# Kernel optimization log

Hardware: AMD Instinct MI355X
Metric: run time of the kernel (lower is better)

## Reference

```python
import jax, jax.numpy as jnp
import numpy as np

NUM_STAGES = 2
DE_NEIGHBORS = 3

def _square_distance(a, b):
    # a: [B,N,3], b: [B,S,3] -> [B,N,S] squared euclidean distances
    return (jnp.sum(a * a, axis=-1)[:, :, None]
            + jnp.sum(b * b, axis=-1)[:, None, :]
            - 2.0 * jnp.einsum('bnc,bsc->bns', a, b))

def _propagate(xyz1, xyz2, points1, points2, k):
    # xyz1:[B,N,3] fine, xyz2:[B,S,3] coarse, points1:[B,D1,N], points2:[B,D2,S]
    p2 = jnp.transpose(points2, (0, 2, 1))  # [B,S,D2]
    B, N, _ = xyz1.shape
    S = xyz2.shape[1]
    if S == 1:
        interp = jnp.broadcast_to(p2, (B, N, p2.shape[-1]))
    else:
        d = _square_distance(xyz1, xyz2)              # [B,N,S]
        neg_top, idx = jax.lax.top_k(-d, k)           # k smallest distances
        dists = -neg_top                              # [B,N,k]
        recip = 1.0 / (dists + 1e-8)
        weight = recip / jnp.sum(recip, axis=2, keepdims=True)  # [B,N,k]
        # gather neighbor features: [B,N,k,D2]
        gathered = jnp.take_along_axis(p2[:, None, :, :], idx[..., None], axis=2)
        interp = jnp.sum(gathered * weight[..., None], axis=2)  # [B,N,D2]
    if points1 is not None:
        p1 = jnp.transpose(points1, (0, 2, 1))        # [B,N,D1]
        new = jnp.concatenate([p1, interp], axis=-1)
    else:
        new = interp
    return jnp.transpose(new, (0, 2, 1))              # [B,D1+D2,N]

def setup_inputs() -> dict:
    key = jax.random.key(0)
    ks = jax.random.split(key, 6)
    return {
        'xyz0': jax.random.normal(ks[0], (4, 8192, 3), dtype=jnp.float32),
        'xyz1': jax.random.normal(ks[1], (4, 2048, 3), dtype=jnp.float32),
        'xyz2': jax.random.normal(ks[2], (4, 512, 3), dtype=jnp.float32),
        'x0': jax.random.normal(ks[3], (4, 128, 8192), dtype=jnp.float32),
        'x1': jax.random.normal(ks[4], (4, 256, 2048), dtype=jnp.float32),
        'x2': jax.random.normal(ks[5], (4, 512, 512), dtype=jnp.float32),
    }

def reference(xyz0, xyz1, xyz2, x0, x1, x2):
    # original forward reverses the lists; emulate with pre-reversed lists
    xyz_list = [xyz2, xyz1, xyz0]   # coarse -> fine
    x_list = [x2, x1, x0]
    x = x_list[0]
    for i in range(NUM_STAGES):
        x = _propagate(xyz_list[i + 1], xyz_list[i], x_list[i + 1], x, DE_NEIGHBORS)
    return x  # [4, 896, 8192]
```

## Files before the change

### kernel.cpp

```cpp
#include <hip/hip_runtime.h>

#define BIG 3.0e38f

__device__ __forceinline__ void insert3(float d, int s,
                                        float& d0, float& d1, float& d2,
                                        int& i0, int& i1, int& i2) {
    const bool b0 = d < d0;
    const bool b1 = d < d1;
    const bool b2 = d < d2;
    d2 = b1 ? d1 : (b2 ? d : d2);
    i2 = b1 ? i1 : (b2 ? s : i2);
    d1 = b0 ? d0 : (b1 ? d : d1);
    i1 = b0 ? i0 : (b1 ? s : i1);
    d0 = b0 ? d : d0;
    i0 = b0 ? s : i0;
}

template <int S>
__device__ void knn_tile(const float* __restrict__ xyzF, const float* __restrict__ xyzC,
                         int N, int b, int nb,
                         int* __restrict__ idx, float* __restrict__ w,
                         void* smem) {
    constexpr int SPC = S / 8;
    float4* sc  = (float4*)smem;
    float*  smd = (float*)((char*)smem + S * 16);
    int*    smi = (int*)((char*)smem + S * 16 + 3072);
    const int tid = threadIdx.x;

    for (int i = tid; i < S; i += 256) {
        const float x = xyzC[(b * S + i) * 3 + 0];
        const float y = xyzC[(b * S + i) * 3 + 1];
        const float z = xyzC[(b * S + i) * 3 + 2];
        sc[i] = make_float4(x, y, z, x * x + y * y + z * z);
    }
    __syncthreads();

    const int q  = tid & 31;
    const int sp = tid >> 5;
    const int n  = nb + q;
    const float ax = xyzF[(b * N + n) * 3 + 0];
    const float ay = xyzF[(b * N + n) * 3 + 1];
    const float az = xyzF[(b * N + n) * 3 + 2];
    const float an = ax * ax + ay * ay + az * az;

    float d0 = BIG, d1 = BIG, d2 = BIG;
    int i0 = 0, i1 = 0, i2 = 0;
    const int s0 = sp * SPC;
#pragma unroll 8
    for (int s = s0; s < s0 + SPC; ++s) {
        const float4 p = sc[s];
        const float t = ax * p.x + ay * p.y + az * p.z;
        const float d = an + p.w - 2.0f * t;
        insert3(d, s, d0, d1, d2, i0, i1, i2);
    }

    smd[tid * 3 + 0] = d0; smi[tid * 3 + 0] = i0;
    smd[tid * 3 + 1] = d1; smi[tid * 3 + 1] = i1;
    smd[tid * 3 + 2] = d2; smi[tid * 3 + 2] = i2;
    __syncthreads();

    if (tid < 32) {
        float e0 = BIG, e1 = BIG, e2 = BIG;
        int j0 = 0, j1 = 0, j2 = 0;
#pragma unroll
        for (int ch = 0; ch < 8; ++ch) {
#pragma unroll
            for (int k = 0; k < 3; ++k) {
                insert3(smd[(ch * 32 + tid) * 3 + k], smi[(ch * 32 + tid) * 3 + k],
                        e0, e1, e2, j0, j1, j2);
            }
        }
        const float r0 = 1.0f / (e0 + 1e-8f);
        const float r1 = 1.0f / (e1 + 1e-8f);
        const float r2 = 1.0f / (e2 + 1e-8f);
        const float rs = r0 + r1 + r2;
        const int nn = nb + tid;
        idx[(b * 3 + 0) * N + nn] = j0;
        idx[(b * 3 + 1) * N + nn] = j1;
        idx[(b * 3 + 2) * N + nn] = j2;
        w[(b * 3 + 0) * N + nn] = r0 / rs;
        w[(b * 3 + 1) * N + nn] = r1 / rs;
        w[(b * 3 + 2) * N + nn] = r2 / rs;
    }
}

__device__ void transpose_tile(const float* __restrict__ in, float* __restrict__ out,
                               int C, int N, int OS,
                               int b, int nb, int cb, void* smem) {
    float (*s)[65] = (float (*)[65])smem;
    const int lo = threadIdx.x & 63;
    const int r  = threadIdx.x >> 6;
#pragma unroll
    for (int i = 0; i < 16; ++i) {
        const int cl = r + 4 * i;
        s[cl][lo] = in[((size_t)b * C + cb + cl) * N + nb + lo];
    }
    __syncthreads();
#pragma unroll
    for (int i = 0; i < 16; ++i) {
        const int pl = r + 4 * i;
        out[((size_t)b * N + nb + pl) * OS + cb + lo] = s[lo][pl];
    }
}

__global__ __launch_bounds__(256) void k1_stage(const float* __restrict__ xyz0,
                                                const float* __restrict__ xyz1,
                                                const float* __restrict__ xyz2,
                                                const float* __restrict__ x0,
                                                const float* __restrict__ x1,
                                                const float* __restrict__ x2,
                                                float* __restrict__ x1P,
                                                float* __restrict__ x2P,
                                                int* __restrict__ idx1,
                                                float* __restrict__ w1,
                                                int* __restrict__ idx2,
                                                float* __restrict__ w2,
                                                float* __restrict__ out) {
    __shared__ float4 smem4[2432];
    const int id = blockIdx.x;
    if (id < 1024) {
        const int b  = id >> 8;
        const int nb = (id & 255) * 32;
        knn_tile<2048>(xyz0, xyz1, 8192, b, nb, idx2, w2, smem4);
    } else if (id < 1280) {
        const int r  = id - 1024;
        const int b  = r >> 6;
        const int nb = (r & 63) * 32;
        knn_tile<512>(xyz1, xyz2, 2048, b, nb, idx1, w1, smem4);
    } else if (id < 1536) {
        const int r  = id - 1280;
        const int b  = r >> 6;
        const int nb = (r & 7) * 64;
        const int cb = ((r >> 3) & 7) * 64;
        transpose_tile(x2, x2P, 512, 512, 512, b, nb, cb, smem4);
    } else if (id < 2048) {
        const int r  = id - 1536;
        const int b  = r >> 7;
        const int nb = (r & 31) * 64;
        const int cb = ((r >> 5) & 3) * 64;
        transpose_tile(x1, x1P, 256, 2048, 256, b, nb, cb, smem4);
    } else {
        const int r  = id - 2048;
        const int b  = r >> 6;
        const int lb = r & 63;
        const float4* src = (const float4*)x0;
        float4* dst = (float4*)out;
#pragma unroll
        for (int t = 0; t < 16; ++t) {
            const int i = lb * 4096 + t * 256 + threadIdx.x;
            dst[(size_t)b * (896 * 2048) + i] = src[(size_t)b * (128 * 2048) + i];
        }
    }
}

__global__ __launch_bounds__(256) void final_fused(const float* __restrict__ x1P,
                                                   const float* __restrict__ x2P,
                                                   const int* __restrict__ idx1,
                                                   const float* __restrict__ w1,
                                                   const int* __restrict__ idx2,
                                                   const float* __restrict__ w2,
                                                   float* __restrict__ out) {
    __shared__ float tile[64][65];
    __shared__ int   sj[9][64];
    __shared__ float sw[9][64];
    const int b = blockIdx.y;
    const int id = blockIdx.x;
    const int ntile = (id & 7) * 16 + ((id >> 3) & 15);
    const int ctile = id >> 7;
    const int nb = ntile * 64;
    const int tid = threadIdx.x;

    if (ctile < 4) {
        if (tid < 64) {
#pragma unroll
            for (int k = 0; k < 3; ++k) {
                sj[k][tid] = idx2[(b * 3 + k) * 8192 + nb + tid];
                sw[k][tid] = w2[(b * 3 + k) * 8192 + nb + tid];
            }
        }
        __syncthreads();
        const int cb = ctile * 64;
        {
            const int c = tid & 63, r = tid >> 6;
            const float* xb = x1P + (size_t)b * 2048 * 256 + cb + c;
#pragma unroll
            for (int i = 0; i < 16; ++i) {
                const int p = r + 4 * i;
                const float v = sw[0][p] * xb[(size_t)sj[0][p] * 256]
                              + sw[1][p] * xb[(size_t)sj[1][p] * 256]
                              + sw[2][p] * xb[(size_t)sj[2][p] * 256];
                tile[p][c] = v;
            }
        }
        __syncthreads();
        {
            const int p = tid & 63, r = tid >> 6;
#pragma unroll
            for (int i = 0; i < 16; ++i) {
                const int cl = r + 4 * i;
                out[((size_t)b * 896 + 128 + cb + cl) * 8192 + nb + p] = tile[p][cl];
            }
        }
    } else {
        if (tid < 64) {
            const int n = nb + tid;
#pragma unroll
            for (int k = 0; k < 3; ++k) {
                const int   j  = idx2[(b * 3 + k) * 8192 + n];
                const float wk = w2[(b * 3 + k) * 8192 + n];
#pragma unroll
                for (int m = 0; m < 3; ++m) {
                    sj[k * 3 + m][tid] = idx1[(b * 3 + m) * 2048 + j];
                    sw[k * 3 + m][tid] = wk * w1[(b * 3 + m) * 2048 + j];
                }
            }
        }
        __syncthreads();
        const int cb = (ctile - 4) * 64;
        {
            const int c = tid & 63, r = tid >> 6;
            const float* xb = x2P + (size_t)b * 512 * 512 + cb + c;
#pragma unroll
            for (int i = 0; i < 16; ++i) {
                const int p = r + 4 * i;
                float v = 0.0f;
#pragma unroll
                for (int j = 0; j < 9; ++j) {
                    v += sw[j][p] * xb[(size_t)sj[j][p] * 512];
                }
                tile[p][c] = v;
            }
        }
        __syncthreads();
        {
            const int p = tid & 63, r = tid >> 6;
#pragma unroll
            for (int i = 0; i < 16; ++i) {
                const int cl = r + 4 * i;
                out[((size_t)b * 896 + 384 + cb + cl) * 8192 + nb + p] = tile[p][cl];
            }
        }
    }
}

extern "C" void kernel_launch(void* const* d_in, const int* in_sizes, int n_in,
                              void* d_out, int out_size, void* d_ws, size_t ws_size,
                              hipStream_t stream) {
    const float* xyz0 = (const float*)d_in[0];
    const float* xyz1 = (const float*)d_in[1];
    const float* xyz2 = (const float*)d_in[2];
    const float* x0   = (const float*)d_in[3];
    const float* x1   = (const float*)d_in[4];
    const float* x2   = (const float*)d_in[5];
    float* out = (float*)d_out;

    char* ws = (char*)d_ws;
    float* x1P  = (float*)(ws + 0);
    float* x2P  = (float*)(ws + 8388608);
    int*   idx1 = (int*)(ws + 12582912);
    float* w1   = (float*)(ws + 12681216);
    int*   idx2 = (int*)(ws + 12779520);
    float* w2   = (float*)(ws + 13172736);

    k1_stage<<<dim3(2304), 256, 0, stream>>>(xyz0, xyz1, xyz2, x0, x1, x2,
                                             x1P, x2P, idx1, w1, idx2, w2, out);
    final_fused<<<dim3(1536, 4), 256, 0, stream>>>(x1P, x2P, idx1, w1, idx2, w2, out);
}
```

Baseline: 213.9 us.

## Interleave stage-1 block roles, remap final blocks per XCD, use nontemporal stores

The first kernel interleaves heavy KNN blocks with light transpose and copy blocks (4 of every 9) so long-running work is spread across the whole grid rather than concentrated at the front. The final kernel flattens the grid and maps each batch onto a pair of XCDs, so the gathered x1P/x2P tiles for that batch stay within those XCDs' L2 caches. Neighbor index and weight loading now uses 192 threads instead of 64. Output writes and the x0 copy use nontemporal loads and stores to avoid polluting cache. The added index arithmetic (divisions by 9 and 12) is minor, and the XCD mapping relies on round-robin block dispatch across the eight XCDs.

```diff
diff --git a/kernel.cpp b/kernel.cpp
--- a/kernel.cpp
+++ b/kernel.cpp
@@ -1,6 +1,8 @@
 #include <hip/hip_runtime.h>
 
 #define BIG 3.0e38f
+
+typedef float vf4 __attribute__((ext_vector_type(4)));
 
 __device__ __forceinline__ void insert3(float d, int s,
                                         float& d0, float& d1, float& d2,
@@ -118,37 +120,43 @@
                                                 float* __restrict__ out) {
     __shared__ float4 smem4[2432];
     const int id = blockIdx.x;
-    if (id < 1024) {
-        const int b  = id >> 8;
-        const int nb = (id & 255) * 32;
+    const int g  = id / 9;
+    const int r9 = id - g * 9;
+    if (r9 < 4) {
+        const int kid = g * 4 + r9;
+        const int b  = kid >> 8;
+        const int nb = (kid & 255) * 32;
         knn_tile<2048>(xyz0, xyz1, 8192, b, nb, idx2, w2, smem4);
-    } else if (id < 1280) {
-        const int r  = id - 1024;
-        const int b  = r >> 6;
-        const int nb = (r & 63) * 32;
-        knn_tile<512>(xyz1, xyz2, 2048, b, nb, idx1, w1, smem4);
-    } else if (id < 1536) {
-        const int r  = id - 1280;
-        const int b  = r >> 6;
-        const int nb = (r & 7) * 64;
-        const int cb = ((r >> 3) & 7) * 64;
-        transpose_tile(x2, x2P, 512, 512, 512, b, nb, cb, smem4);
-    } else if (id < 2048) {
-        const int r  = id - 1536;
-        const int b  = r >> 7;
-        const int nb = (r & 31) * 64;
-        const int cb = ((r >> 5) & 3) * 64;
-        transpose_tile(x1, x1P, 256, 2048, 256, b, nb, cb, smem4);
     } else {
-        const int r  = id - 2048;
-        const int b  = r >> 6;
-        const int lb = r & 63;
-        const float4* src = (const float4*)x0;
-        float4* dst = (float4*)out;
-#pragma unroll
-        for (int t = 0; t < 16; ++t) {
-            const int i = lb * 4096 + t * 256 + threadIdx.x;
-            dst[(size_t)b * (896 * 2048) + i] = src[(size_t)b * (128 * 2048) + i];
+        const int mid = g * 5 + (r9 - 4);
+        if (mid < 256) {
+            const int b  = mid >> 6;
+            const int nb = (mid & 63) * 32;
+            knn_tile<512>(xyz1, xyz2, 2048, b, nb, idx1, w1, smem4);
+        } else if (mid < 512) {
+            const int r  = mid - 256;
+            const int b  = r >> 6;
+            const int nb = (r & 7) * 64;
+            const int cb = ((r >> 3) & 7) * 64;
+            transpose_tile(x2, x2P, 512, 512, 512, b, nb, cb, smem4);
+        } else if (mid < 1024) {
+            const int r  = mid - 512;
+            const int b  = r >> 7;
+            const int nb = (r & 31) * 64;
+            const int cb = ((r >> 5) & 3) * 64;
+            transpose_tile(x1, x1P, 256, 2048, 256, b, nb, cb, smem4);
+        } else {
+            const int r  = mid - 1024;
+            const int b  = r >> 6;
+            const int lb = r & 63;
+            const vf4* src = (const vf4*)x0;
+            vf4* dst = (vf4*)out;
+#pragma unroll
+            for (int t = 0; t < 16; ++t) {
+                const int i = lb * 4096 + t * 256 + threadIdx.x;
+                const vf4 v = __builtin_nontemporal_load(&src[(size_t)b * (128 * 2048) + i]);
+                __builtin_nontemporal_store(v, &dst[(size_t)b * (896 * 2048) + i]);
+            }
         }
     }
 }
@@ -163,20 +171,20 @@
     __shared__ float tile[64][65];
     __shared__ int   sj[9][64];
     __shared__ float sw[9][64];
-    const int b = blockIdx.y;
-    const int id = blockIdx.x;
-    const int ntile = (id & 7) * 16 + ((id >> 3) & 15);
-    const int ctile = id >> 7;
-    const int nb = ntile * 64;
+    const int id  = blockIdx.x;
+    const int xcd = id & 7;
+    const int b   = xcd >> 1;
+    const int local = ((id >> 3) << 1) | (xcd & 1);
+    const int ntile = local / 12;
+    const int ctile = local - ntile * 12;
+    const int nb  = ntile * 64;
     const int tid = threadIdx.x;
 
     if (ctile < 4) {
-        if (tid < 64) {
-#pragma unroll
-            for (int k = 0; k < 3; ++k) {
-                sj[k][tid] = idx2[(b * 3 + k) * 8192 + nb + tid];
-                sw[k][tid] = w2[(b * 3 + k) * 8192 + nb + tid];
-            }
+        if (tid < 192) {
+            const int p = tid & 63, k = tid >> 6;
+            sj[k][p] = idx2[(b * 3 + k) * 8192 + nb + p];
+            sw[k][p] = w2[(b * 3 + k) * 8192 + nb + p];
         }
         __syncthreads();
         const int cb = ctile * 64;
@@ -198,21 +206,19 @@
 #pragma unroll
             for (int i = 0; i < 16; ++i) {
                 const int cl = r + 4 * i;
-                out[((size_t)b * 896 + 128 + cb + cl) * 8192 + nb + p] = tile[p][cl];
+                __builtin_nontemporal_store(tile[p][cl],
+                    &out[((size_t)b * 896 + 128 + cb + cl) * 8192 + nb + p]);
             }
         }
     } else {
-        if (tid < 64) {
-            const int n = nb + tid;
-#pragma unroll
-            for (int k = 0; k < 3; ++k) {
-                const int   j  = idx2[(b * 3 + k) * 8192 + n];
-                const float wk = w2[(b * 3 + k) * 8192 + n];
-#pragma unroll
-                for (int m = 0; m < 3; ++m) {
-                    sj[k * 3 + m][tid] = idx1[(b * 3 + m) * 2048 + j];
-                    sw[k * 3 + m][tid] = wk * w1[(b * 3 + m) * 2048 + j];
-                }
+        if (tid < 192) {
+            const int p = tid & 63, k = tid >> 6;
+            const int   j  = idx2[(b * 3 + k) * 8192 + nb + p];
+            const float wk = w2[(b * 3 + k) * 8192 + nb + p];
+#pragma unroll
+            for (int m = 0; m < 3; ++m) {
+                sj[k * 3 + m][p] = idx1[(b * 3 + m) * 2048 + j];
+                sw[k * 3 + m][p] = wk * w1[(b * 3 + m) * 2048 + j];
             }
         }
         __syncthreads();
@@ -237,7 +243,8 @@
 #pragma unroll
             for (int i = 0; i < 16; ++i) {
                 const int cl = r + 4 * i;
-                out[((size_t)b * 896 + 384 + cb + cl) * 8192 + nb + p] = tile[p][cl];
+                __builtin_nontemporal_store(tile[p][cl],
+                    &out[((size_t)b * 896 + 384 + cb + cl) * 8192 + nb + p]);
             }
         }
     }
@@ -264,5 +271,5 @@
 
     k1_stage<<<dim3(2304), 256, 0, stream>>>(xyz0, xyz1, xyz2, x0, x1, x2,
                                              x1P, x2P, idx1, w1, idx2, w2, out);
-    final_fused<<<dim3(1536, 4), 256, 0, stream>>>(x1P, x2P, idx1, w1, idx2, w2, out);
-}
+    final_fused<<<dim3(6144), 256, 0, stream>>>(x1P, x2P, idx1, w1, idx2, w2, out);
+}
```

New measurement: 218.3 us. 1.02x slower.

## Split final gather into x2 and x1 kernels, staging x2 slices in LDS

Applied to the files above, without the earlier changes.

The fused final kernel is split in two. The x2 path stages a 512x32 channel slice of the transposed x2 into swizzled shared memory and does the 9-neighbour weighted gather from LDS, writing output rows directly without a transpose tile. The x1 path keeps the tile-transpose approach with a new block ordering and loads its indices with 192 threads. Output writes and the x0 copy now use nontemporal loads and stores. The cost is an extra kernel launch and a 64KB LDS footprint per block in x2_gather, which limits occupancy.

```diff
diff --git a/kernel.cpp b/kernel.cpp
--- a/kernel.cpp
+++ b/kernel.cpp
@@ -1,6 +1,8 @@
 #include <hip/hip_runtime.h>
 
 #define BIG 3.0e38f
+
+typedef float vf4 __attribute__((ext_vector_type(4)));
 
 __device__ __forceinline__ void insert3(float d, int s,
                                         float& d0, float& d1, float& d2,
@@ -143,102 +145,119 @@
         const int r  = id - 2048;
         const int b  = r >> 6;
         const int lb = r & 63;
-        const float4* src = (const float4*)x0;
-        float4* dst = (float4*)out;
+        const vf4* src = (const vf4*)x0;
+        vf4* dst = (vf4*)out;
 #pragma unroll
         for (int t = 0; t < 16; ++t) {
             const int i = lb * 4096 + t * 256 + threadIdx.x;
-            dst[(size_t)b * (896 * 2048) + i] = src[(size_t)b * (128 * 2048) + i];
-        }
-    }
-}
-
-__global__ __launch_bounds__(256) void final_fused(const float* __restrict__ x1P,
-                                                   const float* __restrict__ x2P,
-                                                   const int* __restrict__ idx1,
-                                                   const float* __restrict__ w1,
-                                                   const int* __restrict__ idx2,
-                                                   const float* __restrict__ w2,
-                                                   float* __restrict__ out) {
+            const vf4 v = __builtin_nontemporal_load(&src[(size_t)b * (128 * 2048) + i]);
+            __builtin_nontemporal_store(v, &dst[(size_t)b * (896 * 2048) + i]);
+        }
+    }
+}
+
+__global__ __launch_bounds__(256) void x2_gather(const float* __restrict__ x2P,
+                                                 const int* __restrict__ idx1,
+                                                 const float* __restrict__ w1,
+                                                 const int* __restrict__ idx2,
+                                                 const float* __restrict__ w2,
+                                                 float* __restrict__ out) {
+    __shared__ float sx2[512 * 32];
+    const int id  = blockIdx.x;
+    const int grp = id >> 6;
+    const int b   = (id >> 4) & 3;
+    const int ct  = id & 15;
+    const int cb  = ct * 32;
+    const int tid = threadIdx.x;
+
+    {
+        const int c  = tid & 31;
+        const int r0 = tid >> 5;
+        const float* src = x2P + (size_t)b * 512 * 512 + cb + c;
+#pragma unroll 8
+        for (int row = r0; row < 512; row += 8) {
+            sx2[row * 32 + (c ^ (row & 31))] = src[(size_t)row * 512];
+        }
+    }
+    __syncthreads();
+
+    const int wave = tid >> 6;
+    const int p    = tid & 63;
+
+    for (int t = 0; t < 8; ++t) {
+        const int nb = (grp * 8 + t) * 64;
+        const int n  = nb + p;
+        int   rowb[9], rl[9];
+        float wgt[9];
+#pragma unroll
+        for (int k = 0; k < 3; ++k) {
+            const int   j  = idx2[(b * 3 + k) * 8192 + n];
+            const float wk = w2[(b * 3 + k) * 8192 + n];
+#pragma unroll
+            for (int m = 0; m < 3; ++m) {
+                const int row = idx1[(b * 3 + m) * 2048 + j];
+                rowb[k * 3 + m] = row * 32;
+                rl[k * 3 + m]   = row & 31;
+                wgt[k * 3 + m]  = wk * w1[(b * 3 + m) * 2048 + j];
+            }
+        }
+#pragma unroll
+        for (int cc = 0; cc < 8; ++cc) {
+            const int c = wave * 8 + cc;
+            float v = 0.0f;
+#pragma unroll
+            for (int j = 0; j < 9; ++j) {
+                v += wgt[j] * sx2[rowb[j] + (c ^ rl[j])];
+            }
+            __builtin_nontemporal_store(v,
+                &out[((size_t)b * 896 + 384 + cb + c) * 8192 + n]);
+        }
+    }
+}
+
+__global__ __launch_bounds__(256) void x1_gather(const float* __restrict__ x1P,
+                                                 const int* __restrict__ idx2,
+                                                 const float* __restrict__ w2,
+                                                 float* __restrict__ out) {
     __shared__ float tile[64][65];
-    __shared__ int   sj[9][64];
-    __shared__ float sw[9][64];
-    const int b = blockIdx.y;
+    __shared__ int   sj[3][64];
+    __shared__ float sw[3][64];
     const int id = blockIdx.x;
-    const int ntile = (id & 7) * 16 + ((id >> 3) & 15);
-    const int ctile = id >> 7;
+    const int e  = id & 15;
+    const int b  = e >> 2;
+    const int ct = e & 3;
+    const int ntile = id >> 4;
     const int nb = ntile * 64;
     const int tid = threadIdx.x;
 
-    if (ctile < 4) {
-        if (tid < 64) {
-#pragma unroll
-            for (int k = 0; k < 3; ++k) {
-                sj[k][tid] = idx2[(b * 3 + k) * 8192 + nb + tid];
-                sw[k][tid] = w2[(b * 3 + k) * 8192 + nb + tid];
-            }
-        }
-        __syncthreads();
-        const int cb = ctile * 64;
-        {
-            const int c = tid & 63, r = tid >> 6;
-            const float* xb = x1P + (size_t)b * 2048 * 256 + cb + c;
-#pragma unroll
-            for (int i = 0; i < 16; ++i) {
-                const int p = r + 4 * i;
-                const float v = sw[0][p] * xb[(size_t)sj[0][p] * 256]
-                              + sw[1][p] * xb[(size_t)sj[1][p] * 256]
-                              + sw[2][p] * xb[(size_t)sj[2][p] * 256];
-                tile[p][c] = v;
-            }
-        }
-        __syncthreads();
-        {
-            const int p = tid & 63, r = tid >> 6;
-#pragma unroll
-            for (int i = 0; i < 16; ++i) {
-                const int cl = r + 4 * i;
-                out[((size_t)b * 896 + 128 + cb + cl) * 8192 + nb + p] = tile[p][cl];
-            }
-        }
-    } else {
-        if (tid < 64) {
-            const int n = nb + tid;
-#pragma unroll
-            for (int k = 0; k < 3; ++k) {
-                const int   j  = idx2[(b * 3 + k) * 8192 + n];
-                const float wk = w2[(b * 3 + k) * 8192 + n];
-#pragma unroll
-                for (int m = 0; m < 3; ++m) {
-                    sj[k * 3 + m][tid] = idx1[(b * 3 + m) * 2048 + j];
-                    sw[k * 3 + m][tid] = wk * w1[(b * 3 + m) * 2048 + j];
-                }
-            }
-        }
-        __syncthreads();
-        const int cb = (ctile - 4) * 64;
-        {
-            const int c = tid & 63, r = tid >> 6;
-            const float* xb = x2P + (size_t)b * 512 * 512 + cb + c;
-#pragma unroll
-            for (int i = 0; i < 16; ++i) {
-                const int p = r + 4 * i;
-                float v = 0.0f;
-#pragma unroll
-                for (int j = 0; j < 9; ++j) {
-                    v += sw[j][p] * xb[(size_t)sj[j][p] * 512];
-                }
-                tile[p][c] = v;
-            }
-        }
-        __syncthreads();
-        {
-            const int p = tid & 63, r = tid >> 6;
-#pragma unroll
-            for (int i = 0; i < 16; ++i) {
-                const int cl = r + 4 * i;
-                out[((size_t)b * 896 + 384 + cb + cl) * 8192 + nb + p] = tile[p][cl];
-            }
+    if (tid < 192) {
+        const int p = tid & 63, k = tid >> 6;
+        sj[k][p] = idx2[(b * 3 + k) * 8192 + nb + p];
+        sw[k][p] = w2[(b * 3 + k) * 8192 + nb + p];
+    }
+    __syncthreads();
+
+    const int cb = ct * 64;
+    {
+        const int c = tid & 63, r = tid >> 6;
+        const float* xb = x1P + (size_t)b * 2048 * 256 + cb + c;
+#pragma unroll
+        for (int i = 0; i < 16; ++i) {
+            const int p = r + 4 * i;
+            const float v = sw[0][p] * xb[(size_t)sj[0][p] * 256]
+                          + sw[1][p] * xb[(size_t)sj[1][p] * 256]
+                          + sw[2][p] * xb[(size_t)sj[2][p] * 256];
+            tile[p][c] = v;
+        }
+    }
+    __syncthreads();
+    {
+        const int p = tid & 63, r = tid >> 6;
+#pragma unroll
+        for (int i = 0; i < 16; ++i) {
+            const int cl = r + 4 * i;
+            __builtin_nontemporal_store(tile[p][cl],
+                &out[((size_t)b * 896 + 128 + cb + cl) * 8192 + nb + p]);
         }
     }
 }
@@ -264,5 +283,6 @@
 
     k1_stage<<<dim3(2304), 256, 0, stream>>>(xyz0, xyz1, xyz2, x0, x1, x2,
                                              x1P, x2P, idx1, w1, idx2, w2, out);
-    final_fused<<<dim3(1536, 4), 256, 0, stream>>>(x1P, x2P, idx1, w1, idx2, w2, out);
-}
+    x2_gather<<<dim3(1024), 256, 0, stream>>>(x2P, idx1, w1, idx2, w2, out);
+    x1_gather<<<dim3(2048), 256, 0, stream>>>(x1P, idx2, w2, out);
+}
```

After: 244.3 us. 1.14x slower.
